# Kernel tuning notes

Measured on AMD Instinct MI355X. Metric: run time of the kernel, lower is better.

The kernel has to match this reference:

```python
import jax, jax.numpy as jnp
import numpy as np

B, TP, TF, C, H, W = 8, 3, 4, 256, 64, 64
BN_EPS = 1e-3  # YOLOX BaseConv BatchNorm2d eps


def setup_inputs() -> dict:
    key = jax.random.key(0)
    ks = jax.random.split(key, 12)
    s = 1.0 / np.sqrt(C)
    return {
        "feature": jax.random.normal(ks[0], (B, TP + 1, C, H, W), jnp.float32),
        "past_time_constant": jax.random.normal(ks[1], (B, TP), jnp.float32),
        "future_time_constant": jax.random.normal(ks[2], (B, TF), jnp.float32),
        # fc_time_constant: Linear(1, C)
        "w_tc": jax.random.normal(ks[3], (C, 1), jnp.float32),
        "b_tc": jax.random.normal(ks[4], (C,), jnp.float32) * 0.1,
        # fc_in: Linear(2C, C)
        "w_in": jax.random.normal(ks[5], (C, 2 * C), jnp.float32) * (1.0 / np.sqrt(2 * C)),
        "b_in": jnp.zeros((C,), jnp.float32),
        # conv_p: 1x1 conv (no bias) + BN + SiLU
        "conv_w": jax.random.normal(ks[6], (C, C), jnp.float32) * s,
        "bn_gamma": jnp.ones((C,), jnp.float32),
        "bn_beta": jnp.zeros((C,), jnp.float32),
        "bn_mean": jax.random.normal(ks[7], (C,), jnp.float32) * 0.1,
        "bn_var": jnp.ones((C,), jnp.float32) + jax.random.uniform(ks[8], (C,)) * 0.1,
        # fc_query / fc_key: Linear(C, C)
        "w_q": jax.random.normal(ks[9], (C, C), jnp.float32) * s,
        "b_q": jnp.zeros((C,), jnp.float32),
        "w_k": jax.random.normal(ks[10], (C, C), jnp.float32) * s,
        "b_k": jnp.zeros((C,), jnp.float32),
        # p_attn: [1,1,C,1,1]
        "p_attn": jnp.ones((1, 1, C, 1, 1), jnp.float32),
    }


def reference(feature, past_time_constant, future_time_constant,
              w_tc, b_tc, w_in, b_in, conv_w, bn_gamma, bn_beta, bn_mean, bn_var,
              w_q, b_q, w_k, b_k, p_attn):
    b, t1, c, h, w = feature.shape
    tp = past_time_constant.shape[1]
    tf = future_time_constant.shape[1]
    silu = jax.nn.silu

    # conv_p = 1x1 conv (bias=False) + BatchNorm(eval) + SiLU, over all TP+1 frames
    x = jnp.einsum('oc,btchw->btohw', conv_w, feature)
    scale = bn_gamma / jnp.sqrt(bn_var + BN_EPS)          # [C]
    x = x * scale[:, None, None] + (bn_beta - bn_mean * scale)[:, None, None]
    feature_p = silu(x)                                    # [B,TP+1,C,H,W]

    # time-constant embeddings: tanh(Linear(1->C))
    ptc = jnp.tanh(past_time_constant[..., None] * w_tc[:, 0] + b_tc)    # [B,TP,C]
    ftc = jnp.tanh(future_time_constant[..., None] * w_tc[:, 0] + b_tc)  # [B,TF,C]

    # past branch: global max+avg pool over HxW, concat, fc_in+SiLU, add ptc
    fp_past = feature_p[:, :-1]                            # [B,TP,C,H,W]
    pool_p = jnp.concatenate([fp_past.max(axis=(-2, -1)), fp_past.mean(axis=(-2, -1))], axis=-1)  # [B,TP,2C]
    attn_in_p = silu(jnp.einsum('oc,btc->bto', w_in, pool_p) + b_in) + ptc  # [B,TP,C]

    # future branch: feature_f = last raw frame broadcast over TF (pool identical per TF)
    last = feature[:, -1]                                  # [B,C,H,W]
    pool_f = jnp.concatenate([last.max(axis=(-2, -1)), last.mean(axis=(-2, -1))], axis=-1)  # [B,2C]
    attn_in_f = silu(pool_f @ w_in.T + b_in)[:, None, :] + ftc  # [B,TF,C]

    q = attn_in_f @ w_q.T + b_q                            # [B,TF,C]
    k = attn_in_p @ w_k.T + b_k                            # [B,TP,C]
    v = (feature_p[:, -1:] - fp_past).reshape(b, tp, c * h * w)  # [B,TP,CHW]

    # NOTE: torch code scales by sqrt(attn_query.size(1)) == sqrt(TF), not sqrt(C)
    attn_w = jnp.einsum('bfc,bpc->bfp', q, k) / jnp.sqrt(jnp.asarray(tf, q.dtype))  # [B,TF,TP]
    attn = jnp.einsum('bfp,bpd->bfd', attn_w, v).reshape(b, tf, c, h, w)

    # residual: feature_f + attn * p_attn / attn_key.size(1) (== TP)
    out = last[:, None] + attn * p_attn / tp               # [B,TF,C,H,W]
    return out
```

## Files before the change

kernel.cpp:

```cpp
#include <hip/hip_runtime.h>

#define B_   8
#define T1_  4
#define TP_  3
#define TF_  4
#define C_   256
#define HW_  4096

#define OFF_FP     0ull
#define OFF_PMAXK  67108864ull
#define OFF_PSUM   67133440ull
#define OFF_RMAX   67158016ull
#define OFF_RSUM   67166208ull
#define OFF_Q      67174400ull
#define OFF_K      67207168ull
#define OFF_AW     67231744ull

typedef __attribute__((ext_vector_type(8))) short bf16x8;
typedef __attribute__((ext_vector_type(4))) float f32x4;

__device__ __forceinline__ unsigned short f2bf(float f) {
    unsigned int u = __float_as_uint(f);
    u += 0x7fffu + ((u >> 16) & 1u);
    return (unsigned short)(u >> 16);
}
__device__ __forceinline__ unsigned int fkey(float x) {
    unsigned int b = __float_as_uint(x);
    return (b & 0x80000000u) ? ~b : (b | 0x80000000u);
}
__device__ __forceinline__ float funkey(unsigned int k) {
    unsigned int b = (k & 0x80000000u) ? (k ^ 0x80000000u) : ~k;
    return __uint_as_float(b);
}
__device__ __forceinline__ float silu_f(float x) { return x / (1.0f + __expf(-x)); }

__device__ __forceinline__ void dec8(uint4 u, float* f) {
    f[0] = __uint_as_float(u.x << 16); f[1] = __uint_as_float(u.x & 0xffff0000u);
    f[2] = __uint_as_float(u.y << 16); f[3] = __uint_as_float(u.y & 0xffff0000u);
    f[4] = __uint_as_float(u.z << 16); f[5] = __uint_as_float(u.z & 0xffff0000u);
    f[6] = __uint_as_float(u.w << 16); f[7] = __uint_as_float(u.w & 0xffff0000u);
}

__global__ __launch_bounds__(256) void k0_rawpool(const float* __restrict__ feature,
                                                  float* __restrict__ rmax,
                                                  float* __restrict__ rsum) {
    const int blk = blockIdx.x;
    const int b = blk >> 8, c = blk & 255;
    const float* base = feature + ((size_t)(b * 4 + 3) * C_ + c) * HW_;
    const int tid = threadIdx.x;
    float mx = -3.4e38f, sm = 0.0f;
    #pragma unroll
    for (int k = 0; k < 4; ++k) {
        float4 v = *(const float4*)(base + (k * 256 + tid) * 4);
        mx = fmaxf(mx, fmaxf(fmaxf(v.x, v.y), fmaxf(v.z, v.w)));
        sm += (v.x + v.y) + (v.z + v.w);
    }
    #pragma unroll
    for (int m = 1; m < 64; m <<= 1) {
        mx = fmaxf(mx, __shfl_xor(mx, m));
        sm += __shfl_xor(sm, m);
    }
    __shared__ float wmx[4], wsm[4];
    const int wave = tid >> 6;
    if ((tid & 63) == 0) { wmx[wave] = mx; wsm[wave] = sm; }
    __syncthreads();
    if (tid == 0) {
        rmax[b * C_ + c] = fmaxf(fmaxf(wmx[0], wmx[1]), fmaxf(wmx[2], wmx[3]));
        rsum[b * C_ + c] = (wsm[0] + wsm[1]) + (wsm[2] + wsm[3]);
    }
}

__global__ __launch_bounds__(256) void k1_conv(
    const float* __restrict__ feature, const float* __restrict__ Wc,
    const float* __restrict__ gamma, const float* __restrict__ beta,
    const float* __restrict__ mean, const float* __restrict__ var,
    unsigned short* __restrict__ fp_out,
    unsigned int* __restrict__ pmaxk, float* __restrict__ psum) {
    __shared__ __align__(16) char smem[34816];
    unsigned short* lds_a = (unsigned short*)smem;
    unsigned short* lds_b = (unsigned short*)(smem + 20480);
    float* s_scale = (float*)(smem + 25600);
    float* s_shift = (float*)(smem + 26624);

    const int tid   = threadIdx.x;
    const int bt    = blockIdx.x >> 6;
    const int hwblk = blockIdx.x & 63;
    const int b = bt >> 2, t = bt & 3;
    const int hw0 = hwblk * 64;
    const int lane = tid & 63;
    const int wave = tid >> 6;
    const int q = lane >> 4;
    const int col = lane & 15;
    const int kg  = tid >> 6;
    const int hwl = tid & 63;

    {
        float sc = gamma[tid] * rsqrtf(var[tid] + 1e-3f);
        s_scale[tid] = sc;
        s_shift[tid] = beta[tid] - mean[tid] * sc;
    }

    const float* Fb = feature + (size_t)bt * C_ * HW_;
    f32x4 acc[4][4] = {};

    for (int k0 = 0; k0 < C_; k0 += 32) {
        __syncthreads();
        #pragma unroll
        for (int it = 0; it < 8; ++it) {
            int p = it * 256 + tid;
            int ol = p >> 3, cq = p & 7;
            float4 v = *(const float4*)(Wc + ol * 256 + k0 + cq * 4);
            ushort4 u;
            u.x = f2bf(v.x); u.y = f2bf(v.y); u.z = f2bf(v.z); u.w = f2bf(v.w);
            *(ushort4*)&lds_a[ol * 40 + cq * 4] = u;
        }
        {
            float fv[8];
            #pragma unroll
            for (int j = 0; j < 8; ++j)
                fv[j] = Fb[(size_t)(k0 + kg * 8 + j) * HW_ + hw0 + hwl];
            uint4 pk;
            pk.x = ((unsigned)f2bf(fv[1]) << 16) | f2bf(fv[0]);
            pk.y = ((unsigned)f2bf(fv[3]) << 16) | f2bf(fv[2]);
            pk.z = ((unsigned)f2bf(fv[5]) << 16) | f2bf(fv[4]);
            pk.w = ((unsigned)f2bf(fv[7]) << 16) | f2bf(fv[6]);
            *(uint4*)&lds_b[hwl * 40 + kg * 8] = pk;
        }
        __syncthreads();
        bf16x8 afr[4], bfr[4];
        #pragma unroll
        for (int mi = 0; mi < 4; ++mi)
            afr[mi] = *(const bf16x8*)&lds_a[(wave * 64 + mi * 16 + col) * 40 + q * 8];
        #pragma unroll
        for (int ni = 0; ni < 4; ++ni)
            bfr[ni] = *(const bf16x8*)&lds_b[(ni * 16 + col) * 40 + q * 8];
        #pragma unroll
        for (int mi = 0; mi < 4; ++mi)
            #pragma unroll
            for (int ni = 0; ni < 4; ++ni)
                acc[mi][ni] = __builtin_amdgcn_mfma_f32_16x16x32_bf16(afr[mi], bfr[ni], acc[mi][ni], 0, 0, 0);
    }

    unsigned short* fpo = fp_out + (size_t)bt * C_ * HW_;
    float pmx_r[16], psm_r[16];
    #pragma unroll
    for (int mi = 0; mi < 4; ++mi) {
        #pragma unroll
        for (int r = 0; r < 4; ++r) {
            const int o = wave * 64 + mi * 16 + q * 4 + r;
            const float sc = s_scale[o], sh = s_shift[o];
            float mx = -3.4e38f, sm = 0.0f;
            #pragma unroll
            for (int ni = 0; ni < 4; ++ni) {
                float x = acc[mi][ni][r] * sc + sh;
                float s = silu_f(x);
                fpo[(size_t)o * HW_ + hw0 + ni * 16 + col] = f2bf(s);
                mx = fmaxf(mx, s);
                sm += s;
            }
            pmx_r[mi * 4 + r] = mx;
            psm_r[mi * 4 + r] = sm;
        }
    }
    if (t < 3) {
        __syncthreads();
        float* pmx = (float*)smem;
        float* psm = (float*)(smem + 17408);
        #pragma unroll
        for (int mi = 0; mi < 4; ++mi)
            #pragma unroll
            for (int r = 0; r < 4; ++r) {
                const int o = wave * 64 + mi * 16 + q * 4 + r;
                pmx[o * 17 + col] = pmx_r[mi * 4 + r];
                psm[o * 17 + col] = psm_r[mi * 4 + r];
            }
        __syncthreads();
        const int o = tid;
        float m = pmx[o * 17], s2 = psm[o * 17];
        #pragma unroll
        for (int cc = 1; cc < 16; ++cc) {
            m = fmaxf(m, pmx[o * 17 + cc]);
            s2 += psm[o * 17 + cc];
        }
        atomicMax(&pmaxk[(b * 3 + t) * C_ + o], fkey(m));
        atomicAdd(&psum[(b * 3 + t) * C_ + o], s2);
    }
}

__global__ __launch_bounds__(256) void k2_vec(
    const float* __restrict__ past_tc, const float* __restrict__ fut_tc,
    const float* __restrict__ w_tc, const float* __restrict__ b_tc,
    const float* __restrict__ w_in, const float* __restrict__ b_in,
    const float* __restrict__ w_q, const float* __restrict__ b_q,
    const float* __restrict__ w_k, const float* __restrict__ b_k,
    const unsigned int* __restrict__ pmaxk, const float* __restrict__ psum,
    const float* __restrict__ rmax, const float* __restrict__ rsum,
    float* __restrict__ qout, float* __restrict__ kout) {
    __shared__ float pool[512];
    __shared__ float avec[256];
    const int b = blockIdx.x / 7;
    const int idx = blockIdx.x % 7;
    const int o = threadIdx.x;
    const bool pside = (idx < 3);
    if (pside) {
        pool[o]       = funkey(pmaxk[(b * 3 + idx) * C_ + o]);
        pool[256 + o] = psum[(b * 3 + idx) * C_ + o] * (1.0f / 4096.0f);
    } else {
        pool[o]       = rmax[b * C_ + o];
        pool[256 + o] = rsum[b * C_ + o] * (1.0f / 4096.0f);
    }
    __syncthreads();
    float s = b_in[o];
    const float* wr = w_in + (size_t)o * 512;
    #pragma unroll 8
    for (int c = 0; c < 512; ++c) s += wr[c] * pool[c];
    float v = silu_f(s);
    float tcin = pside ? past_tc[b * 3 + idx] : fut_tc[b * 4 + (idx - 3)];
    float tc = tanhf(tcin * w_tc[o] + b_tc[o]);
    avec[o] = v + tc;
    __syncthreads();
    if (pside) {
        float s2 = b_k[o];
        const float* wk = w_k + (size_t)o * 256;
        #pragma unroll 8
        for (int c = 0; c < 256; ++c) s2 += wk[c] * avec[c];
        kout[(b * 3 + idx) * C_ + o] = s2;
    } else {
        float s2 = b_q[o];
        const float* wq = w_q + (size_t)o * 256;
        #pragma unroll 8
        for (int c = 0; c < 256; ++c) s2 += wq[c] * avec[c];
        qout[(b * 4 + (idx - 3)) * C_ + o] = s2;
    }
}

__global__ __launch_bounds__(64) void k2_attnw(const float* __restrict__ qv,
                                               const float* __restrict__ kv,
                                               float* __restrict__ aw) {
    const int i = blockIdx.x;
    const int b = i / 12, rr = i % 12, f = rr / 3, p = rr % 3;
    const int lane = threadIdx.x;
    const float* qp = qv + (b * 4 + f) * C_;
    const float* kp = kv + (b * 3 + p) * C_;
    float s = 0.0f;
    #pragma unroll
    for (int j = 0; j < 4; ++j) s += qp[lane + 64 * j] * kp[lane + 64 * j];
    #pragma unroll
    for (int m = 1; m < 64; m <<= 1) s += __shfl_xor(s, m);
    if (lane == 0) aw[b * 12 + rr] = s * 0.5f;
}

__global__ __launch_bounds__(256) void k3_out(
    const float* __restrict__ feature, const unsigned short* __restrict__ fp,
    const float* __restrict__ aw, const float* __restrict__ p_attn,
    float* __restrict__ out) {
    const int idx = blockIdx.x;
    const int b = idx >> 9;
    const int c = (idx >> 1) & 255;
    const int half = idx & 1;
    const int hw = half * 2048 + threadIdx.x * 8;

    float a[12];
    #pragma unroll
    for (int i = 0; i < 12; ++i) a[i] = aw[b * 12 + i];
    const float pa = p_attn[c] * (1.0f / 3.0f);

    const size_t ts = (size_t)C_ * HW_;
    const size_t base = ((size_t)(b * 4) * C_ + c) * HW_ + hw;

    uint4 u0 = *(const uint4*)(fp + base);
    uint4 u1 = *(const uint4*)(fp + base + ts);
    uint4 u2 = *(const uint4*)(fp + base + 2 * ts);
    uint4 u3 = *(const uint4*)(fp + base + 3 * ts);
    float4 l0 = *(const float4*)(feature + base + 3 * ts);
    float4 l1 = *(const float4*)(feature + base + 3 * ts + 4);

    float f0[8], f1[8], f2[8], f3[8];
    dec8(u0, f0); dec8(u1, f1); dec8(u2, f2); dec8(u3, f3);
    float lastv[8] = {l0.x, l0.y, l0.z, l0.w, l1.x, l1.y, l1.z, l1.w};

    float ov[4][8];
    #pragma unroll
    for (int e = 0; e < 8; ++e) {
        float d0 = f3[e] - f0[e];
        float d1 = f3[e] - f1[e];
        float d2 = f3[e] - f2[e];
        #pragma unroll
        for (int f = 0; f < 4; ++f) {
            float at = a[f * 3 + 0] * d0 + a[f * 3 + 1] * d1 + a[f * 3 + 2] * d2;
            ov[f][e] = lastv[e] + at * pa;
        }
    }
    #pragma unroll
    for (int f = 0; f < 4; ++f) {
        size_t ob = ((size_t)(b * 4 + f) * C_ + c) * HW_ + hw;
        *(float4*)(out + ob)     = make_float4(ov[f][0], ov[f][1], ov[f][2], ov[f][3]);
        *(float4*)(out + ob + 4) = make_float4(ov[f][4], ov[f][5], ov[f][6], ov[f][7]);
    }
}

extern "C" void kernel_launch(void* const* d_in, const int* in_sizes, int n_in,
                              void* d_out, int out_size, void* d_ws, size_t ws_size,
                              hipStream_t stream) {
    const float* feature = (const float*)d_in[0];
    const float* past_tc = (const float*)d_in[1];
    const float* fut_tc  = (const float*)d_in[2];
    const float* w_tc    = (const float*)d_in[3];
    const float* b_tc    = (const float*)d_in[4];
    const float* w_in    = (const float*)d_in[5];
    const float* b_in    = (const float*)d_in[6];
    const float* conv_w  = (const float*)d_in[7];
    const float* gamma   = (const float*)d_in[8];
    const float* beta    = (const float*)d_in[9];
    const float* mean    = (const float*)d_in[10];
    const float* var     = (const float*)d_in[11];
    const float* w_q     = (const float*)d_in[12];
    const float* b_q     = (const float*)d_in[13];
    const float* w_k     = (const float*)d_in[14];
    const float* b_k     = (const float*)d_in[15];
    const float* p_attn  = (const float*)d_in[16];

    char* ws = (char*)d_ws;
    unsigned short* fp  = (unsigned short*)(ws + OFF_FP);
    unsigned int* pmaxk = (unsigned int*)(ws + OFF_PMAXK);
    float* psum = (float*)(ws + OFF_PSUM);
    float* rmax = (float*)(ws + OFF_RMAX);
    float* rsum = (float*)(ws + OFF_RSUM);
    float* qout = (float*)(ws + OFF_Q);
    float* kout = (float*)(ws + OFF_K);
    float* aw   = (float*)(ws + OFF_AW);

    hipMemsetAsync(ws + OFF_PMAXK, 0, 49152, stream);

    k0_rawpool<<<B_ * C_, 256, 0, stream>>>(feature, rmax, rsum);
    k1_conv<<<B_ * T1_ * 64, 256, 0, stream>>>(feature, conv_w, gamma, beta, mean, var,
                                               fp, pmaxk, psum);
    k2_vec<<<B_ * 7, 256, 0, stream>>>(past_tc, fut_tc, w_tc, b_tc, w_in, b_in,
                                       w_q, b_q, w_k, b_k, pmaxk, psum, rmax, rsum,
                                       qout, kout);
    k2_attnw<<<B_ * TF_ * TP_, 64, 0, stream>>>(qout, kout, aw);
    k3_out<<<B_ * C_ * 2, 256, 0, stream>>>(feature, fp, aw, p_attn, (float*)d_out);
}
```

Baseline: 362.1 us.

## Pre-convert BN-folded conv weights to bf16 and double-buffer feature tiles

A new prep kernel folds the BatchNorm scale into the conv weights and converts them to bf16 once, instead of every conv block re-reading and converting the fp32 weights into LDS on every K step. The conv kernel now reads A fragments straight from global/L2 and double-buffers the B tile in LDS. The next feature slice is prefetched into registers to overlap loads with MFMA, which leaves one barrier per iteration. The pooling reduction uses wave shuffles and per-lane atomics instead of an LDS transpose, which adds more atomics and relies on L2 hits for the weight fragments.

```diff
diff --git a/kernel.cpp b/kernel.cpp
--- a/kernel.cpp
+++ b/kernel.cpp
@@ -15,6 +15,8 @@
 #define OFF_Q      67174400ull
 #define OFF_K      67207168ull
 #define OFF_AW     67231744ull
+#define OFF_WBF    67232128ull
+#define OFF_SHIFT  67363200ull
 
 typedef __attribute__((ext_vector_type(8))) short bf16x8;
 typedef __attribute__((ext_vector_type(4))) float f32x4;
@@ -39,6 +41,28 @@
     f[2] = __uint_as_float(u.y << 16); f[3] = __uint_as_float(u.y & 0xffff0000u);
     f[4] = __uint_as_float(u.z << 16); f[5] = __uint_as_float(u.z & 0xffff0000u);
     f[6] = __uint_as_float(u.w << 16); f[7] = __uint_as_float(u.w & 0xffff0000u);
+}
+
+__global__ __launch_bounds__(256) void kprep(const float* __restrict__ Wc,
+                                             const float* __restrict__ gamma,
+                                             const float* __restrict__ beta,
+                                             const float* __restrict__ mean,
+                                             const float* __restrict__ var,
+                                             unsigned short* __restrict__ Wbf,
+                                             float* __restrict__ shift) {
+    const int tid = threadIdx.x;
+    const int idx = blockIdx.x * 1024 + tid * 4;
+    const int o = idx >> 8;
+    const float sc = gamma[o] * rsqrtf(var[o] + 1e-3f);
+    float4 v = *(const float4*)(Wc + idx);
+    ushort4 u;
+    u.x = f2bf(v.x * sc); u.y = f2bf(v.y * sc);
+    u.z = f2bf(v.z * sc); u.w = f2bf(v.w * sc);
+    *(ushort4*)(Wbf + idx) = u;
+    if (blockIdx.x == 0) {
+        float s2 = gamma[tid] * rsqrtf(var[tid] + 1e-3f);
+        shift[tid] = beta[tid] - mean[tid] * s2;
+    }
 }
 
 __global__ __launch_bounds__(256) void k0_rawpool(const float* __restrict__ feature,
@@ -71,16 +95,12 @@
 }
 
 __global__ __launch_bounds__(256) void k1_conv(
-    const float* __restrict__ feature, const float* __restrict__ Wc,
-    const float* __restrict__ gamma, const float* __restrict__ beta,
-    const float* __restrict__ mean, const float* __restrict__ var,
+    const float* __restrict__ feature, const unsigned short* __restrict__ Wbf,
+    const float* __restrict__ shift,
     unsigned short* __restrict__ fp_out,
     unsigned int* __restrict__ pmaxk, float* __restrict__ psum) {
-    __shared__ __align__(16) char smem[34816];
-    unsigned short* lds_a = (unsigned short*)smem;
-    unsigned short* lds_b = (unsigned short*)(smem + 20480);
-    float* s_scale = (float*)(smem + 25600);
-    float* s_shift = (float*)(smem + 26624);
+    __shared__ __align__(16) unsigned short lds_b[2][64 * 40];
+    __shared__ float s_shift[256];
 
     const int tid   = threadIdx.x;
     const int bt    = blockIdx.x >> 6;
@@ -91,49 +111,40 @@
     const int wave = tid >> 6;
     const int q = lane >> 4;
     const int col = lane & 15;
-    const int kg  = tid >> 6;
-    const int hwl = tid & 63;
-
-    {
-        float sc = gamma[tid] * rsqrtf(var[tid] + 1e-3f);
-        s_scale[tid] = sc;
-        s_shift[tid] = beta[tid] - mean[tid] * sc;
-    }
+    const int kg  = wave;
+    const int hwl = lane;
+
+    s_shift[tid] = shift[tid];
 
     const float* Fb = feature + (size_t)bt * C_ * HW_;
     f32x4 acc[4][4] = {};
 
-    for (int k0 = 0; k0 < C_; k0 += 32) {
-        __syncthreads();
-        #pragma unroll
-        for (int it = 0; it < 8; ++it) {
-            int p = it * 256 + tid;
-            int ol = p >> 3, cq = p & 7;
-            float4 v = *(const float4*)(Wc + ol * 256 + k0 + cq * 4);
-            ushort4 u;
-            u.x = f2bf(v.x); u.y = f2bf(v.y); u.z = f2bf(v.z); u.w = f2bf(v.w);
-            *(ushort4*)&lds_a[ol * 40 + cq * 4] = u;
-        }
-        {
-            float fv[8];
+    float fv[8];
+    #pragma unroll
+    for (int j = 0; j < 8; ++j)
+        fv[j] = Fb[(size_t)(kg * 8 + j) * HW_ + hw0 + hwl];
+
+    for (int it = 0; it < 8; ++it) {
+        const int k0 = it * 32;
+        uint4 pk;
+        pk.x = ((unsigned)f2bf(fv[1]) << 16) | f2bf(fv[0]);
+        pk.y = ((unsigned)f2bf(fv[3]) << 16) | f2bf(fv[2]);
+        pk.z = ((unsigned)f2bf(fv[5]) << 16) | f2bf(fv[4]);
+        pk.w = ((unsigned)f2bf(fv[7]) << 16) | f2bf(fv[6]);
+        *(uint4*)&lds_b[it & 1][hwl * 40 + kg * 8] = pk;
+        if (it < 7) {
             #pragma unroll
             for (int j = 0; j < 8; ++j)
-                fv[j] = Fb[(size_t)(k0 + kg * 8 + j) * HW_ + hw0 + hwl];
-            uint4 pk;
-            pk.x = ((unsigned)f2bf(fv[1]) << 16) | f2bf(fv[0]);
-            pk.y = ((unsigned)f2bf(fv[3]) << 16) | f2bf(fv[2]);
-            pk.z = ((unsigned)f2bf(fv[5]) << 16) | f2bf(fv[4]);
-            pk.w = ((unsigned)f2bf(fv[7]) << 16) | f2bf(fv[6]);
-            *(uint4*)&lds_b[hwl * 40 + kg * 8] = pk;
+                fv[j] = Fb[(size_t)(k0 + 32 + kg * 8 + j) * HW_ + hw0 + hwl];
         }
         __syncthreads();
         bf16x8 afr[4], bfr[4];
         #pragma unroll
         for (int mi = 0; mi < 4; ++mi)
-            afr[mi] = *(const bf16x8*)&lds_a[(wave * 64 + mi * 16 + col) * 40 + q * 8];
+            afr[mi] = *(const bf16x8*)(Wbf + (size_t)(wave * 64 + mi * 16 + col) * 256 + k0 + q * 8);
         #pragma unroll
         for (int ni = 0; ni < 4; ++ni)
-            bfr[ni] = *(const bf16x8*)&lds_b[(ni * 16 + col) * 40 + q * 8];
+            bfr[ni] = *(const bf16x8*)&lds_b[it & 1][(ni * 16 + col) * 40 + q * 8];
         #pragma unroll
         for (int mi = 0; mi < 4; ++mi)
             #pragma unroll
@@ -148,11 +159,11 @@
         #pragma unroll
         for (int r = 0; r < 4; ++r) {
             const int o = wave * 64 + mi * 16 + q * 4 + r;
-            const float sc = s_scale[o], sh = s_shift[o];
+            const float sh = s_shift[o];
             float mx = -3.4e38f, sm = 0.0f;
             #pragma unroll
             for (int ni = 0; ni < 4; ++ni) {
-                float x = acc[mi][ni][r] * sc + sh;
+                float x = acc[mi][ni][r] + sh;
                 float s = silu_f(x);
                 fpo[(size_t)o * HW_ + hw0 + ni * 16 + col] = f2bf(s);
                 mx = fmaxf(mx, s);
@@ -163,27 +174,26 @@
         }
     }
     if (t < 3) {
-        __syncthreads();
-        float* pmx = (float*)smem;
-        float* psm = (float*)(smem + 17408);
-        #pragma unroll
-        for (int mi = 0; mi < 4; ++mi)
-            #pragma unroll
-            for (int r = 0; r < 4; ++r) {
-                const int o = wave * 64 + mi * 16 + q * 4 + r;
-                pmx[o * 17 + col] = pmx_r[mi * 4 + r];
-                psm[o * 17 + col] = psm_r[mi * 4 + r];
+        #pragma unroll
+        for (int i = 0; i < 16; ++i) {
+            float m = pmx_r[i], s = psm_r[i];
+            #pragma unroll
+            for (int d = 1; d < 16; d <<= 1) {
+                m = fmaxf(m, __shfl_xor(m, d));
+                s += __shfl_xor(s, d);
             }
-        __syncthreads();
-        const int o = tid;
-        float m = pmx[o * 17], s2 = psm[o * 17];
-        #pragma unroll
-        for (int cc = 1; cc < 16; ++cc) {
-            m = fmaxf(m, pmx[o * 17 + cc]);
-            s2 += psm[o * 17 + cc];
-        }
-        atomicMax(&pmaxk[(b * 3 + t) * C_ + o], fkey(m));
-        atomicAdd(&psum[(b * 3 + t) * C_ + o], s2);
+            pmx_r[i] = m; psm_r[i] = s;
+        }
+        if (col == 0) {
+            #pragma unroll
+            for (int mi = 0; mi < 4; ++mi)
+                #pragma unroll
+                for (int r = 0; r < 4; ++r) {
+                    const int o = wave * 64 + mi * 16 + q * 4 + r;
+                    atomicMax(&pmaxk[(b * 3 + t) * C_ + o], fkey(pmx_r[mi * 4 + r]));
+                    atomicAdd(&psum[(b * 3 + t) * C_ + o], psm_r[mi * 4 + r]);
+                }
+        }
     }
 }
 
@@ -329,12 +339,14 @@
     float* qout = (float*)(ws + OFF_Q);
     float* kout = (float*)(ws + OFF_K);
     float* aw   = (float*)(ws + OFF_AW);
+    unsigned short* Wbf = (unsigned short*)(ws + OFF_WBF);
+    float* shift = (float*)(ws + OFF_SHIFT);
 
     hipMemsetAsync(ws + OFF_PMAXK, 0, 49152, stream);
 
+    kprep<<<64, 256, 0, stream>>>(conv_w, gamma, beta, mean, var, Wbf, shift);
     k0_rawpool<<<B_ * C_, 256, 0, stream>>>(feature, rmax, rsum);
-    k1_conv<<<B_ * T1_ * 64, 256, 0, stream>>>(feature, conv_w, gamma, beta, mean, var,
-                                               fp, pmaxk, psum);
+    k1_conv<<<B_ * T1_ * 64, 256, 0, stream>>>(feature, Wbf, shift, fp, pmaxk, psum);
     k2_vec<<<B_ * 7, 256, 0, stream>>>(past_tc, fut_tc, w_tc, b_tc, w_in, b_in,
                                        w_q, b_q, w_k, b_k, pmaxk, psum, rmax, rsum,
                                        qout, kout);
```

Measured after the change: 370.7 us. +2.4%, slower.
